# Kernel optimization log

Measured on AMD Instinct MI355X. Metric: run time of the kernel, lower is better.

Reference implementation:

```python
import math
import jax, jax.numpy as jnp
import numpy as np

# Constants (module-level in original repo; plausible biological values)
LATENCY_EPSILON = 1e-6
HAIR_CELL_COMPRESSION_EXPONENT = 0.3
HAIR_CELL_ADAPTATION_SUPPRESSION = 0.5
AUDITORY_NERVE_ADAPTATION_DECAY = 0.9
AUDITORY_NERVE_ADAPTATION_RATE = 0.1

SAMPLE_RATE = 16000
N_FFT = 512
N_FILTERS = 128
OUTPUT_SIZE = 262144
N_TIMESTEPS = 128
SPARSITY = 0.05
F_MIN, F_MAX = 80.0, 7600.0


def build_filterbank() -> np.ndarray:
    """Mel triangular filterbank, faithful to _create_filterbank (integer bin edges)."""
    hz_to_mel = lambda hz: 2595.0 * math.log10(1.0 + hz / 700.0)
    mel_to_hz = lambda mel: 700.0 * (10.0 ** (mel / 2595.0) - 1.0)
    mel_pts = np.linspace(hz_to_mel(F_MIN), hz_to_mel(F_MAX), N_FILTERS + 2)
    hz_pts = np.array([mel_to_hz(m) for m in mel_pts])
    bins = (hz_pts * N_FFT / SAMPLE_RATE).astype(np.int64)  # .long() truncation
    fb = np.zeros((N_FILTERS, N_FFT // 2 + 1), dtype=np.float32)
    for i in range(N_FILTERS):
        l, c, r = bins[i], bins[i + 1], bins[i + 2]
        for j in range(l, c):
            if c > l:
                fb[i, j] = (j - l) / (c - l)
        for j in range(c, r):
            if r > c:
                fb[i, j] = (r - j) / (r - c)
    return fb


def setup_inputs() -> dict:
    key = jax.random.key(0)
    k_audio, k_w = jax.random.split(key)
    audio = jax.random.normal(k_audio, (SAMPLE_RATE,), dtype=jnp.float32)
    filterbank = jnp.asarray(build_filterbank())  # [n_filters, n_fft//2+1]
    W = jax.random.normal(k_w, (OUTPUT_SIZE, N_FILTERS), dtype=jnp.float32) * 0.02
    b = jnp.zeros((OUTPUT_SIZE,), dtype=jnp.float32)
    adaptation_state = jnp.zeros((N_FILTERS,), dtype=jnp.float32)
    return {"audio": audio, "filterbank": filterbank, "W": W, "b": b,
            "adaptation_state": adaptation_state}


def reference(audio, filterbank, W, b, adaptation_state):
    # Basilar membrane: rfft with n=N_FFT (truncates audio to first N_FFT samples)
    spec = jnp.fft.rfft(audio, n=N_FFT)            # [n_fft//2+1] complex
    magnitude = jnp.abs(spec).astype(jnp.float32)   # [257]
    cochlear = filterbank @ magnitude               # [n_filters]
    # Hair cell compression
    hair = jnp.power(cochlear + LATENCY_EPSILON, HAIR_CELL_COMPRESSION_EXPONENT)
    adapted = jax.nn.relu(hair - adaptation_state * HAIR_CELL_ADAPTATION_SUPPRESSION)
    # Output projection (torch Linear: x @ W.T + b)
    activity = W @ adapted + b                      # [output_size]
    # Latency coding: high activity -> early spike (vectorized scatter)
    a_min, a_max = activity.min(), activity.max()
    norm = (activity - a_min) / (a_max - a_min + 1e-6)
    latencies = ((1.0 - norm) * (N_TIMESTEPS - 1)).astype(jnp.int32)  # [output_size]
    fire = norm > SPARSITY                           # [output_size]
    # spikes[t, n] = fire[n] and latencies[n] == t
    spikes = (latencies[None, :] == jnp.arange(N_TIMESTEPS, dtype=jnp.int32)[:, None]) \
             & fire[None, :]                         # [n_timesteps, output_size] bool
    return spikes
```

## Files before the change

### kernel.cpp

```cpp
#include <hip/hip_runtime.h>
#include <math.h>

#ifndef M_PI
#define M_PI 3.14159265358979323846
#endif

#define N_FFT       512
#define N_BINS      257
#define N_FILTERS   128
#define OUTPUT_SIZE 262144
#define N_TIMESTEPS 128

__device__ __forceinline__ unsigned long long enc_d(double f) {
    unsigned long long u = (unsigned long long)__double_as_longlong(f);
    return (u & 0x8000000000000000ull) ? ~u : (u | 0x8000000000000000ull);
}
__device__ __forceinline__ double dec_d(unsigned long long e) {
    unsigned long long u = (e & 0x8000000000000000ull) ? (e ^ 0x8000000000000000ull) : ~e;
    return __longlong_as_double((long long)u);
}

__global__ __launch_bounds__(256) void k1_frontend(
    const float* __restrict__ audio, const float* __restrict__ fb,
    const float* __restrict__ adapt, double* __restrict__ adapted,
    unsigned long long* __restrict__ minmax)
{
    __shared__ double tw_c[N_FFT];
    __shared__ double tw_s[N_FFT];
    __shared__ double aud[N_FFT];
    __shared__ float  mag[N_BINS];

    const int tid = threadIdx.x;

    for (int m = tid; m < N_FFT; m += 256) {
        double ang = (-2.0 * M_PI * (double)m) / (double)N_FFT;
        double s, c;
        sincos(ang, &s, &c);
        tw_c[m] = c;
        tw_s[m] = s;
        aud[m] = (double)audio[m];
    }
    __syncthreads();

    for (int b = tid; b < N_BINS; b += 256) {
        double re = 0.0, im = 0.0;
        int m = 0;
        for (int n = 0; n < N_FFT; ++n) {
            double a = aud[n];
            re += a * tw_c[m];
            im += a * tw_s[m];
            m = (m + b) & (N_FFT - 1);
        }
        mag[b] = (float)sqrt(re * re + im * im);
    }
    __syncthreads();

    if (tid < N_FILTERS) {
        double acc = 0.0;
        const float* row = fb + tid * N_BINS;
        for (int j = 0; j < N_BINS; ++j)
            acc += (double)row[j] * (double)mag[j];
        double x = acc + 1e-6;
        double p = pow(x, 0.3);
        double a = p - (double)adapt[tid] * 0.5;
        adapted[tid] = a > 0.0 ? a : 0.0;
    }
    if (tid == 0) {
        minmax[0] = 0xFFFFFFFFFFFFFFFFull;
        minmax[1] = 0ull;
    }
}

__global__ __launch_bounds__(256) void k2_gemv(
    const float4* __restrict__ W4, const float* __restrict__ bias,
    const double* __restrict__ adapted, double* __restrict__ activity,
    unsigned long long* __restrict__ minmax)
{
    __shared__ double ad[N_FILTERS];
    __shared__ double red_min[256];
    __shared__ double red_max[256];

    const int tid = threadIdx.x;
    if (tid < N_FILTERS) ad[tid] = adapted[tid];
    __syncthreads();

    const int row = blockIdx.x * 256 + tid;
    const float4* wrow = W4 + (size_t)row * (N_FILTERS / 4);

    double acc = 0.0;
    #pragma unroll 8
    for (int j = 0; j < N_FILTERS / 4; ++j) {
        float4 w = wrow[j];
        const int k = j * 4;
        acc += (double)w.x * ad[k];
        acc += (double)w.y * ad[k + 1];
        acc += (double)w.z * ad[k + 2];
        acc += (double)w.w * ad[k + 3];
    }
    double a = acc + (double)bias[row];
    activity[row] = a;

    red_min[tid] = a;
    red_max[tid] = a;
    __syncthreads();
    for (int s = 128; s > 0; s >>= 1) {
        if (tid < s) {
            red_min[tid] = fmin(red_min[tid], red_min[tid + s]);
            red_max[tid] = fmax(red_max[tid], red_max[tid + s]);
        }
        __syncthreads();
    }
    if (tid == 0) {
        atomicMin(&minmax[0], enc_d(red_min[0]));
        atomicMax(&minmax[1], enc_d(red_max[0]));
    }
}

__global__ __launch_bounds__(256) void k3_spikes(
    const double* __restrict__ activity,
    const unsigned long long* __restrict__ minmax,
    int4* __restrict__ out4)
{
    const int tid = blockIdx.x * 256 + threadIdx.x;
    const double amin = dec_d(minmax[0]);
    const double amax = dec_d(minmax[1]);
    const double denom = (amax - amin) + 1e-6;

    const double ax = activity[4 * tid + 0];
    const double ay = activity[4 * tid + 1];
    const double az = activity[4 * tid + 2];
    const double aw = activity[4 * tid + 3];

    const double nx = (ax - amin) / denom;
    const double ny = (ay - amin) / denom;
    const double nz = (az - amin) / denom;
    const double nw = (aw - amin) / denom;

    const int lx = (int)((1.0 - nx) * 127.0);
    const int ly = (int)((1.0 - ny) * 127.0);
    const int lz = (int)((1.0 - nz) * 127.0);
    const int lw = (int)((1.0 - nw) * 127.0);

    const int vx = (nx > 0.05) ? 1 : 0;
    const int vy = (ny > 0.05) ? 1 : 0;
    const int vz = (nz > 0.05) ? 1 : 0;
    const int vw = (nw > 0.05) ? 1 : 0;

    #pragma unroll 4
    for (int t = 0; t < N_TIMESTEPS; ++t) {
        int4 v;
        v.x = (lx == t) ? vx : 0;
        v.y = (ly == t) ? vy : 0;
        v.z = (lz == t) ? vz : 0;
        v.w = (lw == t) ? vw : 0;
        out4[(size_t)t * (OUTPUT_SIZE / 4) + tid] = v;
    }
}

extern "C" void kernel_launch(void* const* d_in, const int* in_sizes, int n_in,
                              void* d_out, int out_size, void* d_ws, size_t ws_size,
                              hipStream_t stream) {
    (void)in_sizes; (void)n_in; (void)out_size; (void)ws_size;

    const float* audio = (const float*)d_in[0];
    const float* fb    = (const float*)d_in[1];
    const float* W     = (const float*)d_in[2];
    const float* bias  = (const float*)d_in[3];
    const float* adapt = (const float*)d_in[4];
    int* out = (int*)d_out;

    double* activity = (double*)d_ws;
    double* adapted  = activity + OUTPUT_SIZE;
    unsigned long long* minmax =
        (unsigned long long*)(adapted + N_FILTERS);

    k1_frontend<<<1, 256, 0, stream>>>(audio, fb, adapt, adapted, minmax);
    k2_gemv<<<OUTPUT_SIZE / 256, 256, 0, stream>>>(
        (const float4*)W, bias, adapted, activity, minmax);
    k3_spikes<<<(OUTPUT_SIZE / 4) / 256, 256, 0, stream>>>(
        activity, minmax, (int4*)out);
}
```

Baseline: 316.6 us.

## Parallelize DFT across 512 threads, wave-cooperative GEMV, split spike writes over timesteps

The single-block frontend now uses 512 threads, with each DFT bin split into two half-sums that are combined afterwards, shortening the serial critical path. The GEMV assigns each wavefront 64 rows and reads W coalesced across lanes. Dot products and the min/max are reduced with shuffles instead of a shared-memory tree. The spike kernel adds a grid dimension so each block writes a quarter of the timesteps, giving more blocks for the 128MB output write at the cost of re-reading activity four times.

```diff
diff --git a/kernel.cpp b/kernel.cpp
--- a/kernel.cpp
+++ b/kernel.cpp
@@ -20,7 +20,7 @@
     return __longlong_as_double((long long)u);
 }
 
-__global__ __launch_bounds__(256) void k1_frontend(
+__global__ __launch_bounds__(512) void k1_frontend(
     const float* __restrict__ audio, const float* __restrict__ fb,
     const float* __restrict__ adapt, double* __restrict__ adapted,
     unsigned long long* __restrict__ minmax)
@@ -28,41 +28,55 @@
     __shared__ double tw_c[N_FFT];
     __shared__ double tw_s[N_FFT];
     __shared__ double aud[N_FFT];
+    __shared__ double re_p[2 * N_BINS];
+    __shared__ double im_p[2 * N_BINS];
     __shared__ float  mag[N_BINS];
 
     const int tid = threadIdx.x;
 
-    for (int m = tid; m < N_FFT; m += 256) {
-        double ang = (-2.0 * M_PI * (double)m) / (double)N_FFT;
+    if (tid < N_FFT) {
+        double ang = (-2.0 * M_PI * (double)tid) / (double)N_FFT;
         double s, c;
         sincos(ang, &s, &c);
-        tw_c[m] = c;
-        tw_s[m] = s;
-        aud[m] = (double)audio[m];
+        tw_c[tid] = c;
+        tw_s[tid] = s;
+        aud[tid] = (double)audio[tid];
     }
     __syncthreads();
 
-    for (int b = tid; b < N_BINS; b += 256) {
+    for (int w = tid; w < 2 * N_BINS; w += 512) {
+        const int b  = w >> 1;
+        const int n0 = (w & 1) * 256;
         double re = 0.0, im = 0.0;
-        int m = 0;
-        for (int n = 0; n < N_FFT; ++n) {
-            double a = aud[n];
+        #pragma unroll 8
+        for (int j = 0; j < 256; ++j) {
+            const int n = n0 + j;
+            const int m = (b * n) & (N_FFT - 1);
+            const double a = aud[n];
             re += a * tw_c[m];
             im += a * tw_s[m];
-            m = (m + b) & (N_FFT - 1);
         }
-        mag[b] = (float)sqrt(re * re + im * im);
+        re_p[w] = re;
+        im_p[w] = im;
+    }
+    __syncthreads();
+
+    if (tid < N_BINS) {
+        const double re = re_p[2 * tid] + re_p[2 * tid + 1];
+        const double im = im_p[2 * tid] + im_p[2 * tid + 1];
+        mag[tid] = (float)sqrt(re * re + im * im);
     }
     __syncthreads();
 
     if (tid < N_FILTERS) {
         double acc = 0.0;
         const float* row = fb + tid * N_BINS;
+        #pragma unroll 4
         for (int j = 0; j < N_BINS; ++j)
             acc += (double)row[j] * (double)mag[j];
-        double x = acc + 1e-6;
-        double p = pow(x, 0.3);
-        double a = p - (double)adapt[tid] * 0.5;
+        const double x = acc + 1e-6;
+        const double p = pow(x, 0.3);
+        const double a = p - (double)adapt[tid] * 0.5;
         adapted[tid] = a > 0.0 ? a : 0.0;
     }
     if (tid == 0) {
@@ -76,43 +90,47 @@
     const double* __restrict__ adapted, double* __restrict__ activity,
     unsigned long long* __restrict__ minmax)
 {
-    __shared__ double ad[N_FILTERS];
-    __shared__ double red_min[256];
-    __shared__ double red_max[256];
+    const int tid  = threadIdx.x;
+    const int lane = tid & 63;
+    const int gwave = blockIdx.x * 4 + (tid >> 6);
+    const int base_row = gwave * 64;
 
-    const int tid = threadIdx.x;
-    if (tid < N_FILTERS) ad[tid] = adapted[tid];
-    __syncthreads();
+    const int kk = (lane >> 1) * 4;
+    const double A0 = adapted[kk + 0];
+    const double A1 = adapted[kk + 1];
+    const double A2 = adapted[kk + 2];
+    const double A3 = adapted[kk + 3];
 
-    const int row = blockIdx.x * 256 + tid;
-    const float4* wrow = W4 + (size_t)row * (N_FILTERS / 4);
+    const int perm = (lane & 1) * 32 + (lane >> 1);
+    const float4* wp = W4 + (size_t)base_row * (N_FILTERS / 4) + perm;
 
-    double acc = 0.0;
-    #pragma unroll 8
-    for (int j = 0; j < N_FILTERS / 4; ++j) {
-        float4 w = wrow[j];
-        const int k = j * 4;
-        acc += (double)w.x * ad[k];
-        acc += (double)w.y * ad[k + 1];
-        acc += (double)w.z * ad[k + 2];
-        acc += (double)w.w * ad[k + 3];
+    double mn = 1e300, mx = -1e300;
+
+    #pragma unroll 4
+    for (int it = 0; it < 32; ++it) {
+        const float4 w = wp[it * 64];
+        double acc = (double)w.x * A0 + (double)w.y * A1
+                   + (double)w.z * A2 + (double)w.w * A3;
+        acc += __shfl_xor(acc, 2);
+        acc += __shfl_xor(acc, 4);
+        acc += __shfl_xor(acc, 8);
+        acc += __shfl_xor(acc, 16);
+        acc += __shfl_xor(acc, 32);
+        const int row = base_row + it * 2 + (lane & 1);
+        const double a = acc + (double)bias[row];
+        if (lane < 2) activity[row] = a;
+        mn = fmin(mn, a);
+        mx = fmax(mx, a);
     }
-    double a = acc + (double)bias[row];
-    activity[row] = a;
 
-    red_min[tid] = a;
-    red_max[tid] = a;
-    __syncthreads();
-    for (int s = 128; s > 0; s >>= 1) {
-        if (tid < s) {
-            red_min[tid] = fmin(red_min[tid], red_min[tid + s]);
-            red_max[tid] = fmax(red_max[tid], red_max[tid + s]);
-        }
-        __syncthreads();
+    #pragma unroll
+    for (int off = 1; off < 64; off <<= 1) {
+        mn = fmin(mn, __shfl_xor(mn, off));
+        mx = fmax(mx, __shfl_xor(mx, off));
     }
-    if (tid == 0) {
-        atomicMin(&minmax[0], enc_d(red_min[0]));
-        atomicMax(&minmax[1], enc_d(red_max[0]));
+    if (lane == 0) {
+        atomicMin(&minmax[0], enc_d(mn));
+        atomicMax(&minmax[1], enc_d(mx));
     }
 }
 
@@ -126,15 +144,10 @@
     const double amax = dec_d(minmax[1]);
     const double denom = (amax - amin) + 1e-6;
 
-    const double ax = activity[4 * tid + 0];
-    const double ay = activity[4 * tid + 1];
-    const double az = activity[4 * tid + 2];
-    const double aw = activity[4 * tid + 3];
-
-    const double nx = (ax - amin) / denom;
-    const double ny = (ay - amin) / denom;
-    const double nz = (az - amin) / denom;
-    const double nw = (aw - amin) / denom;
+    const double nx = (activity[4 * tid + 0] - amin) / denom;
+    const double ny = (activity[4 * tid + 1] - amin) / denom;
+    const double nz = (activity[4 * tid + 2] - amin) / denom;
+    const double nw = (activity[4 * tid + 3] - amin) / denom;
 
     const int lx = (int)((1.0 - nx) * 127.0);
     const int ly = (int)((1.0 - ny) * 127.0);
@@ -146,8 +159,9 @@
     const int vz = (nz > 0.05) ? 1 : 0;
     const int vw = (nw > 0.05) ? 1 : 0;
 
-    #pragma unroll 4
-    for (int t = 0; t < N_TIMESTEPS; ++t) {
+    const int t0 = blockIdx.y * (N_TIMESTEPS / 4);
+    #pragma unroll 8
+    for (int t = t0; t < t0 + N_TIMESTEPS / 4; ++t) {
         int4 v;
         v.x = (lx == t) ? vx : 0;
         v.y = (ly == t) ? vy : 0;
@@ -174,9 +188,9 @@
     unsigned long long* minmax =
         (unsigned long long*)(adapted + N_FILTERS);
 
-    k1_frontend<<<1, 256, 0, stream>>>(audio, fb, adapt, adapted, minmax);
+    k1_frontend<<<1, 512, 0, stream>>>(audio, fb, adapt, adapted, minmax);
     k2_gemv<<<OUTPUT_SIZE / 256, 256, 0, stream>>>(
         (const float4*)W, bias, adapted, activity, minmax);
-    k3_spikes<<<(OUTPUT_SIZE / 4) / 256, 256, 0, stream>>>(
+    k3_spikes<<<dim3(OUTPUT_SIZE / 4 / 256, 4), 256, 0, stream>>>(
         activity, minmax, (int4*)out);
 }
```

Result: slower. 438.1 us (+38.4%).
